# Kernel optimization log

Hardware: AMD Instinct MI355X
Metric: run time of the kernel (lower is better)

Reference implementation:

```python
import jax, jax.numpy as jnp
import numpy as np

X_DIM, H_DIM, Y_DIM, ROLLOUT = 256, 2048, 256, 4096


def setup_inputs() -> dict:
    key = jax.random.key(0)
    ks = jax.random.split(key, 6)
    inp = {
        "x": jax.random.normal(ks[0], (1, ROLLOUT, X_DIM), dtype=jnp.float32),
        "h": jnp.zeros((H_DIM,), dtype=jnp.float32),
        "Wc": jax.random.normal(ks[1], (X_DIM + H_DIM, H_DIM), dtype=jnp.float32) * 0.01,
        "Wu": jax.random.normal(ks[2], (X_DIM + H_DIM, H_DIM), dtype=jnp.float32) * 0.01,
        "Wr": jax.random.normal(ks[3], (X_DIM + H_DIM, H_DIM), dtype=jnp.float32) * 0.01,
        "bc": jnp.zeros((H_DIM,), dtype=jnp.float32),
        "bu": jnp.zeros((H_DIM,), dtype=jnp.float32),
        "br": jnp.zeros((H_DIM,), dtype=jnp.float32),
        "Wh_y": jax.random.normal(ks[4], (H_DIM, Y_DIM), dtype=jnp.float32) * 0.01,
        "by": jnp.zeros((Y_DIM,), dtype=jnp.float32),
    }
    return inp


def reference(x, h, Wc, Wu, Wr, bc, bu, br, Wh_y, by):
    xs = x[0]  # [T, x_dim]

    def step(hid, xt):
        xc = jnp.concatenate([xt, hid])                      # [x_dim + h_dim]
        Lu = jax.nn.sigmoid(xc @ Wu + bu)                    # update gate
        Lr = jax.nn.sigmoid(xc @ Wr + br)                    # reset gate
        xr = jnp.concatenate([xt, hid * Lr])
        c_tilda = jnp.tanh(xr @ Wc + bc)
        h_new = c_tilda * Lu + hid * (1.0 - Lu)
        y = h_new @ Wh_y + by
        return h_new, y

    h_fin, ys = jax.lax.scan(step, h, xs)  # ys: [T, y_dim]
    return ys, h_fin
```

## Files before the change

### kernel.cpp

```cpp
#include <hip/hip_runtime.h>
#include <hip/hip_bf16.h>

#define TSTEPS 4096
#define XD 256
#define HD 2048
#define YD 256
#define KD 2304
#define NWG 256
#define NT 512

#define WU_OFF 0
#define WR_OFF (8*KD*2)
#define WC_OFF (16*KD*2)
#define WY_OFF (24*KD*2)
#define V1_OFF (WY_OFF + HD*4)
#define V2_OFF (V1_OFF + KD*4)
#define RED_OFF (V2_OFF + KD*4)
#define LDS_BYTES (RED_OFF + 256)

#define HFLAGS_U32 0
#define RFLAGS_U32 8192
#define HGO_U32    16384
#define RGO_U32    16640
#define WS_ZERO_BYTES 67584
#define HB0_OFF 67584
#define HB1_OFF 75776
#define RB0_OFF 83968
#define RB1_OFF 92160

__device__ __forceinline__ float bflo(unsigned u){ return __uint_as_float(u << 16); }
__device__ __forceinline__ float bfhi(unsigned u){ return __uint_as_float(u & 0xffff0000u); }
__device__ __forceinline__ unsigned short f2bf(float f){
  unsigned b = __float_as_uint(f);
  b += 0x7fffu + ((b >> 16) & 1u);
  return (unsigned short)(b >> 16);
}
__device__ __forceinline__ float sigmoidf_(float x){ return 1.0f / (1.0f + __expf(-x)); }

__device__ __forceinline__ void gst32f(float* p, float v){
  __hip_atomic_store(p, v, __ATOMIC_RELAXED, __HIP_MEMORY_SCOPE_AGENT);
}
__device__ __forceinline__ void flagst(unsigned* p, unsigned v){
  __hip_atomic_store(p, v, __ATOMIC_RELAXED, __HIP_MEMORY_SCOPE_AGENT);
}
__device__ __forceinline__ void spinflag(const unsigned* p, unsigned epoch, long* budget){
  while (__hip_atomic_load(p, __ATOMIC_RELAXED, __HIP_MEMORY_SCOPE_AGENT) < epoch) {
    if (--(*budget) < 0) break;
    __builtin_amdgcn_s_sleep(1);
  }
}

__device__ __forceinline__ float4 cohload16(const float4* p){
  float4 r;
  asm volatile("global_load_dwordx4 %0, %1, off sc1\n\t"
               "s_waitcnt vmcnt(0)"
               : "=v"(r) : "v"(p) : "memory");
  return r;
}

__device__ __forceinline__ void relay_wait(unsigned* flags, unsigned* go,
                                           unsigned epoch, int wg, int tid, long* budget){
  if (wg == 0) {
    if (tid >= 1 && tid < NWG) spinflag(flags + tid*32, epoch, budget);
    __syncthreads();
    if (tid < 8) flagst(go + tid*32, epoch);
  } else {
    if (tid == 0) spinflag(go + (wg & 7)*32, epoch, budget);
    __syncthreads();
  }
}

template<int I0, int I1, int STRIDE>
__device__ __forceinline__ void dotacc(const float* v, const unsigned short* wcol,
                                       int lane, float4& acc){
  #pragma unroll
  for (int i = I0; i < I1; ++i) {
    int k = 4 * (lane + STRIDE * i);
    float4 vv = *(const float4*)(v + k);
    uint2  wq = *(const uint2*)(wcol + k);
    acc.x = fmaf(vv.x, bflo(wq.x), acc.x);
    acc.y = fmaf(vv.y, bfhi(wq.x), acc.y);
    acc.z = fmaf(vv.z, bflo(wq.y), acc.z);
    acc.w = fmaf(vv.w, bfhi(wq.y), acc.w);
  }
}

extern "C" __global__ void __launch_bounds__(NT)
gru_persistent(const float* __restrict__ x,  const float* __restrict__ h0,
               const float* __restrict__ Wc, const float* __restrict__ Wu,
               const float* __restrict__ Wr, const float* __restrict__ bc,
               const float* __restrict__ bu, const float* __restrict__ br,
               const float* __restrict__ Wy, const float* __restrict__ by,
               float* __restrict__ out, unsigned* wsu)
{
  extern __shared__ char smem[];
  unsigned short* wuS = (unsigned short*)(smem + WU_OFF);
  unsigned short* wrS = (unsigned short*)(smem + WR_OFF);
  unsigned short* wcS = (unsigned short*)(smem + WC_OFF);
  float* wyS = (float*)(smem + WY_OFF);
  float* v1  = (float*)(smem + V1_OFF);
  float* v2  = (float*)(smem + V2_OFF);
  float* red = (float*)(smem + RED_OFF);

  unsigned* hflags = wsu + HFLAGS_U32;
  unsigned* rflags = wsu + RFLAGS_U32;
  unsigned* hgo    = wsu + HGO_U32;
  unsigned* rgo    = wsu + RGO_U32;
  float* hb[2] = { (float*)((char*)wsu + HB0_OFF), (float*)((char*)wsu + HB1_OFF) };
  float* rb[2] = { (float*)((char*)wsu + RB0_OFF), (float*)((char*)wsu + RB1_OFF) };

  const int wg = blockIdx.x, tid = threadIdx.x;
  const int col0 = 8 * wg;

  for (int idx = tid; idx < 8*KD; idx += NT) {
    int c = idx & 7, k = idx >> 3;
    size_t g = (size_t)k * HD + col0 + c;
    wuS[c*KD + k] = f2bf(Wu[g]);
    wrS[c*KD + k] = f2bf(Wr[g]);
    wcS[c*KD + k] = f2bf(Wc[g]);
  }
  for (int k = tid; k < HD; k += NT) wyS[k] = Wy[(size_t)k * YD + wg];
  if (tid < 8) {
    red[16+tid] = bu[col0+tid];
    red[24+tid] = br[col0+tid];
    red[32+tid] = bc[col0+tid];
  }
  if (tid == 0) red[40] = by[wg];
  __syncthreads();

  long budget = 20000000;

  float4 xpref = make_float4(0.f, 0.f, 0.f, 0.f);
  if (tid < XD/4) xpref = ((const float4*)x)[tid];

  const int hw = tid >> 5, l = tid & 31, c = hw & 7;
  const int w  = tid >> 6, l6 = tid & 63;
  const unsigned short* wcol = ((hw < 8) ? wuS : wrS) + c * KD;
  const unsigned short* ccol = wcS + w * KD;

  for (int t = 0; t < TSTEPS; ++t) {
    if (tid < XD/4) {
      ((float4*)v1)[tid] = xpref;
      ((float4*)v2)[tid] = xpref;
    }
    __syncthreads();

    float4 a1 = make_float4(0.f, 0.f, 0.f, 0.f);
    dotacc<0, 2, 32>(v1, wcol, l, a1);

    if (t == 0) {
      ((float4*)(v1 + XD))[tid] = ((const float4*)h0)[tid];
      __syncthreads();
    } else {
      relay_wait(hflags, hgo, (unsigned)t, wg, tid, &budget);
      float4 hv = cohload16((const float4*)hb[(t+1)&1] + tid);
      ((float4*)(v1 + XD))[tid] = hv;
      __syncthreads();
    }

    dotacc<2, 18, 32>(v1, wcol, l, a1);
    {
      float s = (a1.x + a1.y) + (a1.z + a1.w);
      s += __shfl_xor(s, 16); s += __shfl_xor(s, 8); s += __shfl_xor(s, 4);
      s += __shfl_xor(s, 2);  s += __shfl_xor(s, 1);
      if (l == 0) {
        if (hw < 8) red[c] = sigmoidf_(s + red[16+c]);
        else gst32f(rb[t&1] + col0 + c, sigmoidf_(s + red[24+c]) * v1[XD+col0+c]);
      }
    }
    __syncthreads();
    if (tid == 0) flagst(rflags + wg*32, (unsigned)(t+1));

    {
      int k = 256 * w + 4 * l6;
      float4 hv  = *(const float4*)(v1 + XD + k);
      float4 wy4 = *(const float4*)(wyS + k);
      float ys = fmaf(hv.x, wy4.x, fmaf(hv.y, wy4.y, fmaf(hv.z, wy4.z, hv.w * wy4.w)));
      ys += __shfl_xor(ys, 32); ys += __shfl_xor(ys, 16); ys += __shfl_xor(ys, 8);
      ys += __shfl_xor(ys, 4);  ys += __shfl_xor(ys, 2);  ys += __shfl_xor(ys, 1);
      if (l6 == 0) red[8 + w] = ys;
    }
    if (tid < XD/4 && t + 1 < TSTEPS)
      xpref = ((const float4*)(x + (size_t)(t+1) * XD))[tid];

    relay_wait(rflags, rgo, (unsigned)(t+1), wg, tid, &budget);
    {
      float4 rv = cohload16((const float4*)rb[t&1] + tid);
      ((float4*)(v2 + XD))[tid] = rv;
    }
    __syncthreads();
    if (tid == 0 && t > 0) {
      float y = red[8]+red[9]+red[10]+red[11]+red[12]+red[13]+red[14]+red[15] + red[40];
      out[(size_t)(t-1) * YD + wg] = y;
    }

    {
      float4 a2 = make_float4(0.f, 0.f, 0.f, 0.f);
      dotacc<0, 9, 64>(v2, ccol, l6, a2);
      float s = (a2.x + a2.y) + (a2.z + a2.w);
      s += __shfl_xor(s, 32); s += __shfl_xor(s, 16); s += __shfl_xor(s, 8);
      s += __shfl_xor(s, 4);  s += __shfl_xor(s, 2);  s += __shfl_xor(s, 1);
      if (l6 == 0) {
        float cc = tanhf(s + red[32 + w]);
        float u  = red[w];
        float hp = v1[XD + col0 + w];
        gst32f(hb[t&1] + col0 + w, cc * u + hp * (1.0f - u));
      }
    }
    __syncthreads();
    if (tid == 0) flagst(hflags + wg*32, (unsigned)(t+1));
  }

  relay_wait(hflags, hgo, (unsigned)TSTEPS, wg, tid, &budget);
  {
    float4 hv = cohload16((const float4*)hb[(TSTEPS-1)&1] + tid);
    ((float4*)(v1 + XD))[tid] = hv;
  }
  __syncthreads();
  {
    int k = 256 * w + 4 * l6;
    float4 hv  = *(const float4*)(v1 + XD + k);
    float4 wy4 = *(const float4*)(wyS + k);
    float ys = fmaf(hv.x, wy4.x, fmaf(hv.y, wy4.y, fmaf(hv.z, wy4.z, hv.w * wy4.w)));
    ys += __shfl_xor(ys, 32); ys += __shfl_xor(ys, 16); ys += __shfl_xor(ys, 8);
    ys += __shfl_xor(ys, 4);  ys += __shfl_xor(ys, 2);  ys += __shfl_xor(ys, 1);
    if (l6 == 0) red[8 + w] = ys;
  }
  __syncthreads();
  if (tid == 0) {
    float y = red[8]+red[9]+red[10]+red[11]+red[12]+red[13]+red[14]+red[15] + red[40];
    out[(size_t)(TSTEPS-1) * YD + wg] = y;
  }
  if (tid < 8) out[(size_t)TSTEPS * YD + col0 + tid] = v1[XD + col0 + tid];
}

extern "C" void kernel_launch(void* const* d_in, const int* in_sizes, int n_in,
                              void* d_out, int out_size, void* d_ws, size_t ws_size,
                              hipStream_t stream) {
  const float* x  = (const float*)d_in[0];
  const float* h0 = (const float*)d_in[1];
  const float* Wc = (const float*)d_in[2];
  const float* Wu = (const float*)d_in[3];
  const float* Wr = (const float*)d_in[4];
  const float* bc = (const float*)d_in[5];
  const float* bu = (const float*)d_in[6];
  const float* br = (const float*)d_in[7];
  const float* Wy = (const float*)d_in[8];
  const float* by = (const float*)d_in[9];
  float* out = (float*)d_out;
  unsigned* wsu = (unsigned*)d_ws;

  hipFuncSetAttribute((const void*)gru_persistent,
                      hipFuncAttributeMaxDynamicSharedMemorySize, LDS_BYTES);
  hipMemsetAsync(d_ws, 0, WS_ZERO_BYTES, stream);
  gru_persistent<<<dim3(NWG), dim3(NT), LDS_BYTES, stream>>>(
      x, h0, Wc, Wu, Wr, bc, bu, br, Wy, by, out, wsu);
}
```

Before: 23.79 ms.

## Replace flag relay barrier with tag bits embedded in data values

Replaces the centralized flag-plus-go relay (workgroup 0 gathering per-WG flags, then broadcasting) with per-element epoch tags stored in the two low mantissa bits of each published h and r value. Consumers poll their float4 chunk directly until all four tags match. This removes two relay hops and several __syncthreads per step. The own hidden state is now kept in LDS (red[56..]) and x is double-buffered. The tags slightly perturb the float values (low 2 bits overwritten), and the post-barrier syncthreads are removed, so correctness depends on the tag scheme.

```diff
diff --git a/kernel.cpp b/kernel.cpp
--- a/kernel.cpp
+++ b/kernel.cpp
@@ -13,20 +13,17 @@
 #define WR_OFF (8*KD*2)
 #define WC_OFF (16*KD*2)
 #define WY_OFF (24*KD*2)
-#define V1_OFF (WY_OFF + HD*4)
-#define V2_OFF (V1_OFF + KD*4)
-#define RED_OFF (V2_OFF + KD*4)
+#define XB_OFF (WY_OFF + HD*4)
+#define HBUF_OFF (XB_OFF + 2*XD*4)
+#define ZBUF_OFF (HBUF_OFF + HD*4)
+#define RED_OFF (ZBUF_OFF + HD*4)
 #define LDS_BYTES (RED_OFF + 256)
 
-#define HFLAGS_U32 0
-#define RFLAGS_U32 8192
-#define HGO_U32    16384
-#define RGO_U32    16640
-#define WS_ZERO_BYTES 67584
-#define HB0_OFF 67584
-#define HB1_OFF 75776
-#define RB0_OFF 83968
-#define RB1_OFF 92160
+#define HB0_OFF 0
+#define HB1_OFF 8192
+#define RB0_OFF 16384
+#define RB1_OFF 24576
+#define WS_ZERO_BYTES 32768
 
 __device__ __forceinline__ float bflo(unsigned u){ return __uint_as_float(u << 16); }
 __device__ __forceinline__ float bfhi(unsigned u){ return __uint_as_float(u & 0xffff0000u); }
@@ -37,37 +34,24 @@
 }
 __device__ __forceinline__ float sigmoidf_(float x){ return 1.0f / (1.0f + __expf(-x)); }
 
-__device__ __forceinline__ void gst32f(float* p, float v){
-  __hip_atomic_store(p, v, __ATOMIC_RELAXED, __HIP_MEMORY_SCOPE_AGENT);
-}
-__device__ __forceinline__ void flagst(unsigned* p, unsigned v){
-  __hip_atomic_store(p, v, __ATOMIC_RELAXED, __HIP_MEMORY_SCOPE_AGENT);
-}
-__device__ __forceinline__ void spinflag(const unsigned* p, unsigned epoch, long* budget){
-  while (__hip_atomic_load(p, __ATOMIC_RELAXED, __HIP_MEMORY_SCOPE_AGENT) < epoch) {
+__device__ __forceinline__ void storetag(float* p, float v, unsigned tag){
+  unsigned b = (__float_as_uint(v) & ~3u) | tag;
+  __hip_atomic_store((unsigned*)p, b, __ATOMIC_RELAXED, __HIP_MEMORY_SCOPE_AGENT);
+}
+
+__device__ __forceinline__ float4 pollchunk16(const float4* p, unsigned tag, long* budget){
+  float4 r;
+  for (;;) {
+    asm volatile("global_load_dwordx4 %0, %1, off sc1\n\t"
+                 "s_waitcnt vmcnt(0)"
+                 : "=v"(r) : "v"(p) : "memory");
+    unsigned m = (__float_as_uint(r.x) ^ tag) | (__float_as_uint(r.y) ^ tag)
+               | (__float_as_uint(r.z) ^ tag) | (__float_as_uint(r.w) ^ tag);
+    if ((m & 3u) == 0u) break;
     if (--(*budget) < 0) break;
     __builtin_amdgcn_s_sleep(1);
   }
-}
-
-__device__ __forceinline__ float4 cohload16(const float4* p){
-  float4 r;
-  asm volatile("global_load_dwordx4 %0, %1, off sc1\n\t"
-               "s_waitcnt vmcnt(0)"
-               : "=v"(r) : "v"(p) : "memory");
   return r;
-}
-
-__device__ __forceinline__ void relay_wait(unsigned* flags, unsigned* go,
-                                           unsigned epoch, int wg, int tid, long* budget){
-  if (wg == 0) {
-    if (tid >= 1 && tid < NWG) spinflag(flags + tid*32, epoch, budget);
-    __syncthreads();
-    if (tid < 8) flagst(go + tid*32, epoch);
-  } else {
-    if (tid == 0) spinflag(go + (wg & 7)*32, epoch, budget);
-    __syncthreads();
-  }
 }
 
 template<int I0, int I1, int STRIDE>
@@ -97,15 +81,12 @@
   unsigned short* wuS = (unsigned short*)(smem + WU_OFF);
   unsigned short* wrS = (unsigned short*)(smem + WR_OFF);
   unsigned short* wcS = (unsigned short*)(smem + WC_OFF);
-  float* wyS = (float*)(smem + WY_OFF);
-  float* v1  = (float*)(smem + V1_OFF);
-  float* v2  = (float*)(smem + V2_OFF);
-  float* red = (float*)(smem + RED_OFF);
-
-  unsigned* hflags = wsu + HFLAGS_U32;
-  unsigned* rflags = wsu + RFLAGS_U32;
-  unsigned* hgo    = wsu + HGO_U32;
-  unsigned* rgo    = wsu + RGO_U32;
+  float* wyS   = (float*)(smem + WY_OFF);
+  float* xb    = (float*)(smem + XB_OFF);
+  float* hbufS = (float*)(smem + HBUF_OFF);
+  float* zbufS = (float*)(smem + ZBUF_OFF);
+  float* red   = (float*)(smem + RED_OFF);
+
   float* hb[2] = { (float*)((char*)wsu + HB0_OFF), (float*)((char*)wsu + HB1_OFF) };
   float* rb[2] = { (float*)((char*)wsu + RB0_OFF), (float*)((char*)wsu + RB1_OFF) };
 
@@ -124,6 +105,7 @@
     red[16+tid] = bu[col0+tid];
     red[24+tid] = br[col0+tid];
     red[32+tid] = bc[col0+tid];
+    red[56+tid] = h0[col0+tid];
   }
   if (tid == 0) red[40] = by[wg];
   __syncthreads();
@@ -139,41 +121,36 @@
   const unsigned short* ccol = wcS + w * KD;
 
   for (int t = 0; t < TSTEPS; ++t) {
-    if (tid < XD/4) {
-      ((float4*)v1)[tid] = xpref;
-      ((float4*)v2)[tid] = xpref;
+    float* xcur = xb + (t & 1) * XD;
+    if (tid < XD/4) ((float4*)xcur)[tid] = xpref;
+
+    if (t == 0) {
+      ((float4*)hbufS)[tid] = ((const float4*)h0)[tid];
+    } else {
+      float4 hv = pollchunk16((const float4*)hb[(t+1)&1] + tid,
+                              (unsigned)(t & 3), &budget);
+      ((float4*)hbufS)[tid] = hv;
     }
     __syncthreads();
 
     float4 a1 = make_float4(0.f, 0.f, 0.f, 0.f);
-    dotacc<0, 2, 32>(v1, wcol, l, a1);
-
-    if (t == 0) {
-      ((float4*)(v1 + XD))[tid] = ((const float4*)h0)[tid];
-      __syncthreads();
-    } else {
-      relay_wait(hflags, hgo, (unsigned)t, wg, tid, &budget);
-      float4 hv = cohload16((const float4*)hb[(t+1)&1] + tid);
-      ((float4*)(v1 + XD))[tid] = hv;
-      __syncthreads();
-    }
-
-    dotacc<2, 18, 32>(v1, wcol, l, a1);
+    dotacc<0, 2, 32>(xcur, wcol, l, a1);
+    dotacc<0, 16, 32>(hbufS, wcol + XD, l, a1);
     {
       float s = (a1.x + a1.y) + (a1.z + a1.w);
       s += __shfl_xor(s, 16); s += __shfl_xor(s, 8); s += __shfl_xor(s, 4);
       s += __shfl_xor(s, 2);  s += __shfl_xor(s, 1);
       if (l == 0) {
         if (hw < 8) red[c] = sigmoidf_(s + red[16+c]);
-        else gst32f(rb[t&1] + col0 + c, sigmoidf_(s + red[24+c]) * v1[XD+col0+c]);
+        else storetag(rb[t&1] + col0 + c,
+                      sigmoidf_(s + red[24+c]) * red[56+c],
+                      (unsigned)((t+1) & 3));
       }
     }
-    __syncthreads();
-    if (tid == 0) flagst(rflags + wg*32, (unsigned)(t+1));
 
     {
       int k = 256 * w + 4 * l6;
-      float4 hv  = *(const float4*)(v1 + XD + k);
+      float4 hv  = *(const float4*)(hbufS + k);
       float4 wy4 = *(const float4*)(wyS + k);
       float ys = fmaf(hv.x, wy4.x, fmaf(hv.y, wy4.y, fmaf(hv.z, wy4.z, hv.w * wy4.w)));
       ys += __shfl_xor(ys, 32); ys += __shfl_xor(ys, 16); ys += __shfl_xor(ys, 8);
@@ -183,12 +160,13 @@
     if (tid < XD/4 && t + 1 < TSTEPS)
       xpref = ((const float4*)(x + (size_t)(t+1) * XD))[tid];
 
-    relay_wait(rflags, rgo, (unsigned)(t+1), wg, tid, &budget);
-    {
-      float4 rv = cohload16((const float4*)rb[t&1] + tid);
-      ((float4*)(v2 + XD))[tid] = rv;
+    {
+      float4 rv = pollchunk16((const float4*)rb[t&1] + tid,
+                              (unsigned)((t+1) & 3), &budget);
+      ((float4*)zbufS)[tid] = rv;
     }
     __syncthreads();
+
     if (tid == 0 && t > 0) {
       float y = red[8]+red[9]+red[10]+red[11]+red[12]+red[13]+red[14]+red[15] + red[40];
       out[(size_t)(t-1) * YD + wg] = y;
@@ -196,30 +174,31 @@
 
     {
       float4 a2 = make_float4(0.f, 0.f, 0.f, 0.f);
-      dotacc<0, 9, 64>(v2, ccol, l6, a2);
+      dotacc<0, 1, 64>(xcur, ccol, l6, a2);
+      dotacc<0, 8, 64>(zbufS, ccol + XD, l6, a2);
       float s = (a2.x + a2.y) + (a2.z + a2.w);
       s += __shfl_xor(s, 32); s += __shfl_xor(s, 16); s += __shfl_xor(s, 8);
       s += __shfl_xor(s, 4);  s += __shfl_xor(s, 2);  s += __shfl_xor(s, 1);
       if (l6 == 0) {
         float cc = tanhf(s + red[32 + w]);
         float u  = red[w];
-        float hp = v1[XD + col0 + w];
-        gst32f(hb[t&1] + col0 + w, cc * u + hp * (1.0f - u));
+        float hp = red[56 + w];
+        float hn = cc * u + hp * (1.0f - u);
+        red[56 + w] = hn;
+        storetag(hb[t&1] + col0 + w, hn, (unsigned)((t+1) & 3));
       }
     }
-    __syncthreads();
-    if (tid == 0) flagst(hflags + wg*32, (unsigned)(t+1));
-  }
-
-  relay_wait(hflags, hgo, (unsigned)TSTEPS, wg, tid, &budget);
+  }
+
   {
-    float4 hv = cohload16((const float4*)hb[(TSTEPS-1)&1] + tid);
-    ((float4*)(v1 + XD))[tid] = hv;
+    float4 hv = pollchunk16((const float4*)hb[(TSTEPS-1)&1] + tid,
+                            (unsigned)(TSTEPS & 3), &budget);
+    ((float4*)hbufS)[tid] = hv;
   }
   __syncthreads();
   {
     int k = 256 * w + 4 * l6;
-    float4 hv  = *(const float4*)(v1 + XD + k);
+    float4 hv  = *(const float4*)(hbufS + k);
     float4 wy4 = *(const float4*)(wyS + k);
     float ys = fmaf(hv.x, wy4.x, fmaf(hv.y, wy4.y, fmaf(hv.z, wy4.z, hv.w * wy4.w)));
     ys += __shfl_xor(ys, 32); ys += __shfl_xor(ys, 16); ys += __shfl_xor(ys, 8);
@@ -231,7 +210,7 @@
     float y = red[8]+red[9]+red[10]+red[11]+red[12]+red[13]+red[14]+red[15] + red[40];
     out[(size_t)(TSTEPS-1) * YD + wg] = y;
   }
-  if (tid < 8) out[(size_t)TSTEPS * YD + col0 + tid] = v1[XD + col0 + tid];
+  if (tid < 8) out[(size_t)TSTEPS * YD + col0 + tid] = red[56 + tid];
 }
 
 extern "C" void kernel_launch(void* const* d_in, const int* in_sizes, int n_in,
```

Measured after the change: 31.59 ms. +32.8%, slower.

## Move update gate off critical path and fan out per-wave go flags

Applied to the files above, without the earlier changes.

The update-gate dot product and the y projection now run inside the window while waiting for the reset-gate barrier, so the critical path before publishing r only computes the reset gate, using all 8 waves instead of 8 half-waves. The go flags are spread over 64 lines so each wave spins on its own flag, which removes the block-wide barrier after the wait on non-hub workgroups. The hub workgroup issues its coherent load asynchronously and overlaps it with the window work. The x contribution is kept in registers rather than copied to LDS. The per-step critical path gets shorter, in exchange for more flag-polling traffic and more complex synchronisation.

```diff
diff --git a/kernel.cpp b/kernel.cpp
--- a/kernel.cpp
+++ b/kernel.cpp
@@ -13,20 +13,20 @@
 #define WR_OFF (8*KD*2)
 #define WC_OFF (16*KD*2)
 #define WY_OFF (24*KD*2)
-#define V1_OFF (WY_OFF + HD*4)
-#define V2_OFF (V1_OFF + KD*4)
-#define RED_OFF (V2_OFF + KD*4)
+#define HBUF_OFF (WY_OFF + HD*4)
+#define ZBUF_OFF (HBUF_OFF + HD*4)
+#define RED_OFF (ZBUF_OFF + HD*4)
 #define LDS_BYTES (RED_OFF + 256)
 
 #define HFLAGS_U32 0
 #define RFLAGS_U32 8192
 #define HGO_U32    16384
-#define RGO_U32    16640
-#define WS_ZERO_BYTES 67584
-#define HB0_OFF 67584
-#define HB1_OFF 75776
-#define RB0_OFF 83968
-#define RB1_OFF 92160
+#define RGO_U32    18432
+#define WS_ZERO_BYTES 81920
+#define HB0_OFF 81920
+#define HB1_OFF 90112
+#define RB0_OFF 98304
+#define RB1_OFF 106496
 
 __device__ __forceinline__ float bflo(unsigned u){ return __uint_as_float(u << 16); }
 __device__ __forceinline__ float bfhi(unsigned u){ return __uint_as_float(u & 0xffff0000u); }
@@ -57,17 +57,22 @@
                : "=v"(r) : "v"(p) : "memory");
   return r;
 }
-
-__device__ __forceinline__ void relay_wait(unsigned* flags, unsigned* go,
-                                           unsigned epoch, int wg, int tid, long* budget){
-  if (wg == 0) {
-    if (tid >= 1 && tid < NWG) spinflag(flags + tid*32, epoch, budget);
-    __syncthreads();
-    if (tid < 8) flagst(go + tid*32, epoch);
-  } else {
-    if (tid == 0) spinflag(go + (wg & 7)*32, epoch, budget);
-    __syncthreads();
-  }
+__device__ __forceinline__ float4 cohload16_issue(const float4* p){
+  float4 r;
+  asm volatile("global_load_dwordx4 %0, %1, off sc1"
+               : "=v"(r) : "v"(p) : "memory");
+  return r;
+}
+
+__device__ __forceinline__ void hub_wait(unsigned* flags, unsigned* go,
+                                         unsigned epoch, int tid, long* budget){
+  if (tid >= 1 && tid < NWG) spinflag(flags + tid*32, epoch, budget);
+  __syncthreads();
+  if (tid < 64) flagst(go + tid*32, epoch);
+}
+__device__ __forceinline__ void wave_wait(unsigned* go, unsigned epoch,
+                                          int line, int l6, long* budget){
+  if (l6 == 0) spinflag(go + line*32, epoch, budget);
 }
 
 template<int I0, int I1, int STRIDE>
@@ -85,6 +90,22 @@
   }
 }
 
+__device__ __forceinline__ void xpart(const float4 xq, const unsigned short* wcol,
+                                      int l6, float4& acc){
+  uint2 wq = *(const uint2*)(wcol + 4*l6);
+  acc.x = fmaf(xq.x, bflo(wq.x), acc.x);
+  acc.y = fmaf(xq.y, bfhi(wq.x), acc.y);
+  acc.z = fmaf(xq.z, bflo(wq.y), acc.z);
+  acc.w = fmaf(xq.w, bfhi(wq.y), acc.w);
+}
+
+__device__ __forceinline__ float redux64(float4 a){
+  float s = (a.x + a.y) + (a.z + a.w);
+  s += __shfl_xor(s, 32); s += __shfl_xor(s, 16); s += __shfl_xor(s, 8);
+  s += __shfl_xor(s, 4);  s += __shfl_xor(s, 2);  s += __shfl_xor(s, 1);
+  return s;
+}
+
 extern "C" __global__ void __launch_bounds__(NT)
 gru_persistent(const float* __restrict__ x,  const float* __restrict__ h0,
                const float* __restrict__ Wc, const float* __restrict__ Wu,
@@ -97,10 +118,10 @@
   unsigned short* wuS = (unsigned short*)(smem + WU_OFF);
   unsigned short* wrS = (unsigned short*)(smem + WR_OFF);
   unsigned short* wcS = (unsigned short*)(smem + WC_OFF);
-  float* wyS = (float*)(smem + WY_OFF);
-  float* v1  = (float*)(smem + V1_OFF);
-  float* v2  = (float*)(smem + V2_OFF);
-  float* red = (float*)(smem + RED_OFF);
+  float* wyS   = (float*)(smem + WY_OFF);
+  float* hbufS = (float*)(smem + HBUF_OFF);
+  float* zbufS = (float*)(smem + ZBUF_OFF);
+  float* red   = (float*)(smem + RED_OFF);
 
   unsigned* hflags = wsu + HFLAGS_U32;
   unsigned* rflags = wsu + RFLAGS_U32;
@@ -130,98 +151,101 @@
 
   long budget = 20000000;
 
-  float4 xpref = make_float4(0.f, 0.f, 0.f, 0.f);
-  if (tid < XD/4) xpref = ((const float4*)x)[tid];
-
-  const int hw = tid >> 5, l = tid & 31, c = hw & 7;
   const int w  = tid >> 6, l6 = tid & 63;
-  const unsigned short* wcol = ((hw < 8) ? wuS : wrS) + c * KD;
+  const int goline = ((wg & 7) << 3) + w;
+  const unsigned short* ucol = wuS + w * KD;
+  const unsigned short* rcol = wrS + w * KD;
   const unsigned short* ccol = wcS + w * KD;
 
+  float4 xq = ((const float4*)x)[l6];
+  float ureg = 0.f;
+
+  auto window = [&](int t){
+    float4 au = make_float4(0.f, 0.f, 0.f, 0.f);
+    xpart(xq, ucol, l6, au);
+    dotacc<1, 9, 64>(hbufS - XD, ucol, l6, au);
+    ureg = sigmoidf_(redux64(au) + red[16 + w]);
+    int k = 256 * w + 4 * l6;
+    float4 hv4 = *(const float4*)(hbufS + k);
+    float4 wy4 = *(const float4*)(wyS + k);
+    float ys = fmaf(hv4.x, wy4.x, fmaf(hv4.y, wy4.y, fmaf(hv4.z, wy4.z, hv4.w * wy4.w)));
+    ys += __shfl_xor(ys, 32); ys += __shfl_xor(ys, 16); ys += __shfl_xor(ys, 8);
+    ys += __shfl_xor(ys, 4);  ys += __shfl_xor(ys, 2);  ys += __shfl_xor(ys, 1);
+    if (l6 == 0) red[8 + w] = ys;
+    if (t + 1 < TSTEPS) xq = ((const float4*)(x + (size_t)(t+1) * XD))[l6];
+  };
+
   for (int t = 0; t < TSTEPS; ++t) {
-    if (tid < XD/4) {
-      ((float4*)v1)[tid] = xpref;
-      ((float4*)v2)[tid] = xpref;
-    }
-    __syncthreads();
-
     float4 a1 = make_float4(0.f, 0.f, 0.f, 0.f);
-    dotacc<0, 2, 32>(v1, wcol, l, a1);
+    xpart(xq, rcol, l6, a1);
 
     if (t == 0) {
-      ((float4*)(v1 + XD))[tid] = ((const float4*)h0)[tid];
-      __syncthreads();
+      ((float4*)hbufS)[tid] = ((const float4*)h0)[tid];
     } else {
-      relay_wait(hflags, hgo, (unsigned)t, wg, tid, &budget);
+      if (wg == 0) hub_wait(hflags, hgo, (unsigned)t, tid, &budget);
+      else         wave_wait(hgo, (unsigned)t, goline, l6, &budget);
       float4 hv = cohload16((const float4*)hb[(t+1)&1] + tid);
-      ((float4*)(v1 + XD))[tid] = hv;
-      __syncthreads();
-    }
-
-    dotacc<2, 18, 32>(v1, wcol, l, a1);
+      ((float4*)hbufS)[tid] = hv;
+    }
+    __syncthreads();
+
+    dotacc<1, 9, 64>(hbufS - XD, rcol, l6, a1);
     {
-      float s = (a1.x + a1.y) + (a1.z + a1.w);
-      s += __shfl_xor(s, 16); s += __shfl_xor(s, 8); s += __shfl_xor(s, 4);
-      s += __shfl_xor(s, 2);  s += __shfl_xor(s, 1);
-      if (l == 0) {
-        if (hw < 8) red[c] = sigmoidf_(s + red[16+c]);
-        else gst32f(rb[t&1] + col0 + c, sigmoidf_(s + red[24+c]) * v1[XD+col0+c]);
-      }
+      float s = redux64(a1);
+      if (l6 == 0)
+        gst32f(rb[t&1] + col0 + w,
+               sigmoidf_(s + red[24 + w]) * hbufS[col0 + w]);
     }
     __syncthreads();
     if (tid == 0) flagst(rflags + wg*32, (unsigned)(t+1));
 
-    {
-      int k = 256 * w + 4 * l6;
-      float4 hv  = *(const float4*)(v1 + XD + k);
-      float4 wy4 = *(const float4*)(wyS + k);
-      float ys = fmaf(hv.x, wy4.x, fmaf(hv.y, wy4.y, fmaf(hv.z, wy4.z, hv.w * wy4.w)));
-      ys += __shfl_xor(ys, 32); ys += __shfl_xor(ys, 16); ys += __shfl_xor(ys, 8);
-      ys += __shfl_xor(ys, 4);  ys += __shfl_xor(ys, 2);  ys += __shfl_xor(ys, 1);
-      if (l6 == 0) red[8 + w] = ys;
-    }
-    if (tid < XD/4 && t + 1 < TSTEPS)
-      xpref = ((const float4*)(x + (size_t)(t+1) * XD))[tid];
-
-    relay_wait(rflags, rgo, (unsigned)(t+1), wg, tid, &budget);
-    {
-      float4 rv = cohload16((const float4*)rb[t&1] + tid);
-      ((float4*)(v2 + XD))[tid] = rv;
-    }
-    __syncthreads();
+    float4 a2 = make_float4(0.f, 0.f, 0.f, 0.f);
+    xpart(xq, ccol, l6, a2);
+
+    float4 rv;
+    if (wg != 0) {
+      window(t);
+      wave_wait(rgo, (unsigned)(t+1), goline, l6, &budget);
+      rv = cohload16((const float4*)rb[t&1] + tid);
+    } else {
+      hub_wait(rflags, rgo, (unsigned)(t+1), tid, &budget);
+      rv = cohload16_issue((const float4*)rb[t&1] + tid);
+      window(t);
+      asm volatile("s_waitcnt vmcnt(0)" ::: "memory");
+    }
+    ((float4*)zbufS)[tid] = rv;
+    __syncthreads();
+
     if (tid == 0 && t > 0) {
       float y = red[8]+red[9]+red[10]+red[11]+red[12]+red[13]+red[14]+red[15] + red[40];
       out[(size_t)(t-1) * YD + wg] = y;
     }
 
+    dotacc<1, 9, 64>(zbufS - XD, ccol, l6, a2);
     {
-      float4 a2 = make_float4(0.f, 0.f, 0.f, 0.f);
-      dotacc<0, 9, 64>(v2, ccol, l6, a2);
-      float s = (a2.x + a2.y) + (a2.z + a2.w);
-      s += __shfl_xor(s, 32); s += __shfl_xor(s, 16); s += __shfl_xor(s, 8);
-      s += __shfl_xor(s, 4);  s += __shfl_xor(s, 2);  s += __shfl_xor(s, 1);
+      float s = redux64(a2);
       if (l6 == 0) {
         float cc = tanhf(s + red[32 + w]);
-        float u  = red[w];
-        float hp = v1[XD + col0 + w];
-        gst32f(hb[t&1] + col0 + w, cc * u + hp * (1.0f - u));
+        float hp = hbufS[col0 + w];
+        gst32f(hb[t&1] + col0 + w, cc * ureg + hp * (1.0f - ureg));
       }
     }
     __syncthreads();
     if (tid == 0) flagst(hflags + wg*32, (unsigned)(t+1));
   }
 
-  relay_wait(hflags, hgo, (unsigned)TSTEPS, wg, tid, &budget);
+  if (wg == 0) hub_wait(hflags, hgo, (unsigned)TSTEPS, tid, &budget);
+  else         wave_wait(hgo, (unsigned)TSTEPS, goline, l6, &budget);
   {
     float4 hv = cohload16((const float4*)hb[(TSTEPS-1)&1] + tid);
-    ((float4*)(v1 + XD))[tid] = hv;
+    ((float4*)hbufS)[tid] = hv;
   }
   __syncthreads();
   {
     int k = 256 * w + 4 * l6;
-    float4 hv  = *(const float4*)(v1 + XD + k);
+    float4 hv4 = *(const float4*)(hbufS + k);
     float4 wy4 = *(const float4*)(wyS + k);
-    float ys = fmaf(hv.x, wy4.x, fmaf(hv.y, wy4.y, fmaf(hv.z, wy4.z, hv.w * wy4.w)));
+    float ys = fmaf(hv4.x, wy4.x, fmaf(hv4.y, wy4.y, fmaf(hv4.z, wy4.z, hv4.w * wy4.w)));
     ys += __shfl_xor(ys, 32); ys += __shfl_xor(ys, 16); ys += __shfl_xor(ys, 8);
     ys += __shfl_xor(ys, 4);  ys += __shfl_xor(ys, 2);  ys += __shfl_xor(ys, 1);
     if (l6 == 0) red[8 + w] = ys;
@@ -231,7 +255,7 @@
     float y = red[8]+red[9]+red[10]+red[11]+red[12]+red[13]+red[14]+red[15] + red[40];
     out[(size_t)(TSTEPS-1) * YD + wg] = y;
   }
-  if (tid < 8) out[(size_t)TSTEPS * YD + col0 + tid] = v1[XD + col0 + tid];
+  if (tid < 8) out[(size_t)TSTEPS * YD + col0 + tid] = hbufS[col0 + tid];
 }
 
 extern "C" void kernel_launch(void* const* d_in, const int* in_sizes, int n_in,
```

Result: faster. 21.17 ms (-11.0%).
